# Kernel optimization log

Hardware: AMD Instinct MI355X
Metric: run time of the kernel (lower is better)

Reference implementation:

```python
import jax, jax.numpy as jnp
import numpy as np

DIM = 512
HEADS = 8
WIN = 64
HIDDEN = 2048
EPS = 1e-5


def layernorm(x, g, b):
    mu = jnp.mean(x, axis=-1, keepdims=True)
    var = jnp.var(x, axis=-1, keepdims=True)
    return (x - mu) * jax.lax.rsqrt(var + EPS) * g + b


def setup_inputs() -> dict:
    key = jax.random.key(0)
    ks = jax.random.split(key, 10)
    s = lambda fan_in: 1.0 / np.sqrt(fan_in)
    return {
        "x": jax.random.normal(ks[0], (8, 4096, DIM), dtype=jnp.float32),
        "ln1_g": jnp.ones((DIM,), jnp.float32),
        "ln1_b": jnp.zeros((DIM,), jnp.float32),
        "qkv_w": jax.random.normal(ks[1], (DIM, 3 * DIM), jnp.float32) * s(DIM),
        "qkv_b": jnp.zeros((3 * DIM,), jnp.float32),
        "proj_w": jax.random.normal(ks[2], (DIM, DIM), jnp.float32) * s(DIM),
        "proj_b": jnp.zeros((DIM,), jnp.float32),
        "ln2_g": jnp.ones((DIM,), jnp.float32),
        "ln2_b": jnp.zeros((DIM,), jnp.float32),
        "fc1_w": jax.random.normal(ks[3], (DIM, HIDDEN), jnp.float32) * s(DIM),
        "fc1_b": jnp.zeros((HIDDEN,), jnp.float32),
        "fc2_w": jax.random.normal(ks[4], (HIDDEN, DIM), jnp.float32) * s(HIDDEN),
        "fc2_b": jnp.zeros((DIM,), jnp.float32),
    }


def reference(x, ln1_g, ln1_b, qkv_w, qkv_b, proj_w, proj_b, ln2_g, ln2_b,
              fc1_w, fc1_b, fc2_w, fc2_b):
    B, N, C = x.shape
    hd = C // HEADS
    scale = hd ** -0.5

    # --- W-MSA (shift_size forced to 0, attn_mask None) ---
    h = layernorm(x, ln1_g, ln1_b)
    hw = h.reshape(B * (N // WIN), WIN, C)
    qkv = hw @ qkv_w + qkv_b
    qkv = qkv.reshape(-1, WIN, 3, HEADS, hd)
    q = qkv[:, :, 0] * scale
    k = qkv[:, :, 1]
    v = qkv[:, :, 2]
    attn = jnp.einsum('bqhd,bkhd->bhqk', q, k)
    attn = jax.nn.softmax(attn, axis=-1)
    o = jnp.einsum('bhqk,bkhd->bqhd', attn, v).reshape(-1, WIN, C)
    o = o @ proj_w + proj_b
    x = x + o.reshape(B, N, C)

    # --- MLP (GELU exact, dropout=0) ---
    h2 = layernorm(x, ln2_g, ln2_b)
    h2 = jax.nn.gelu(h2 @ fc1_w + fc1_b, approximate=False)
    x = x + (h2 @ fc2_w + fc2_b)
    return x
```

## Files before the change

### kernel.cpp

```cpp
#include <hip/hip_runtime.h>
#include <hip/hip_bf16.h>
#include <cstdint>

typedef unsigned short U16;
typedef float f32x4 __attribute__((ext_vector_type(4)));
typedef __bf16 bf16x8 __attribute__((ext_vector_type(8)));

#define DEVINL __device__ __forceinline__

DEVINL U16 f2bf(float f) {
    unsigned u = __float_as_uint(f);
    return (U16)((u + 0x7FFFu + ((u >> 16) & 1u)) >> 16);
}
DEVINL float bf2f(U16 s) { return __uint_as_float(((unsigned)s) << 16); }

DEVINL void gld16(const void* g, void* l) {
    __builtin_amdgcn_global_load_lds(
        (const __attribute__((address_space(1))) void*)g,
        (__attribute__((address_space(3))) void*)l, 16, 0, 0);
}

#define MFMA_BF16 __builtin_amdgcn_mfma_f32_16x16x32_bf16

__global__ __launch_bounds__(256) void tcast_kernel(const float* __restrict__ w,
                                                    U16* __restrict__ wt, int K, int N) {
    __shared__ float tile[32][33];
    int n0 = blockIdx.x * 32, k0 = blockIdx.y * 32;
    int tx = threadIdx.x, ty = threadIdx.y;
#pragma unroll
    for (int i = 0; i < 32; i += 8) tile[ty + i][tx] = w[(size_t)(k0 + ty + i) * N + (n0 + tx)];
    __syncthreads();
#pragma unroll
    for (int i = 0; i < 32; i += 8) wt[(size_t)(n0 + ty + i) * K + (k0 + tx)] = f2bf(tile[tx][ty + i]);
}

__global__ __launch_bounds__(256) void ln_kernel(const float* __restrict__ x,
                                                 const float* __restrict__ g,
                                                 const float* __restrict__ b,
                                                 U16* __restrict__ out) {
    int lane = threadIdx.x & 63;
    size_t row = (size_t)blockIdx.x * 4 + (threadIdx.x >> 6);
    const float4* xr = (const float4*)(x + row * 512);
    float4 v0 = xr[lane], v1 = xr[lane + 64];
    float s = (v0.x + v0.y) + (v0.z + v0.w) + (v1.x + v1.y) + (v1.z + v1.w);
    float sq = (v0.x * v0.x + v0.y * v0.y + v0.z * v0.z + v0.w * v0.w) +
               (v1.x * v1.x + v1.y * v1.y + v1.z * v1.z + v1.w * v1.w);
#pragma unroll
    for (int m = 1; m < 64; m <<= 1) { s += __shfl_xor(s, m); sq += __shfl_xor(sq, m); }
    float mu = s * (1.f / 512.f);
    float var = sq * (1.f / 512.f) - mu * mu;
    float rs = rsqrtf(var + 1e-5f);
    const float4* g4 = (const float4*)g;
    const float4* b4 = (const float4*)b;
    float4 gv = g4[lane], bv = b4[lane];
    ushort4 o;
    o.x = f2bf((v0.x - mu) * rs * gv.x + bv.x);
    o.y = f2bf((v0.y - mu) * rs * gv.y + bv.y);
    o.z = f2bf((v0.z - mu) * rs * gv.z + bv.z);
    o.w = f2bf((v0.w - mu) * rs * gv.w + bv.w);
    ((ushort4*)(out + row * 512))[lane] = o;
    gv = g4[lane + 64]; bv = b4[lane + 64];
    o.x = f2bf((v1.x - mu) * rs * gv.x + bv.x);
    o.y = f2bf((v1.y - mu) * rs * gv.y + bv.y);
    o.z = f2bf((v1.z - mu) * rs * gv.z + bv.z);
    o.w = f2bf((v1.w - mu) * rs * gv.w + bv.w);
    ((ushort4*)(out + row * 512))[lane + 64] = o;
}

template <int EPI, int K>
__global__ __launch_bounds__(256, 4) void gemm_rt(const U16* __restrict__ A,
                                                  const U16* __restrict__ Bt,
                                                  const float* __restrict__ bias,
                                                  const float* __restrict__ resid,
                                                  U16* __restrict__ outb,
                                                  float* __restrict__ outf,
                                                  int M, int N, int gridN) {
    __shared__ __align__(16) U16 smem[16384];

    const int tid = threadIdx.x;
    const int lane = tid & 63, wv = tid >> 6;
    const int lo = lane & 15, hi = lane >> 4;
    const int wm = wv >> 1, wn = wv & 1;

    const int nwg = gridDim.x, bid = blockIdx.x;
    const int swzb = (bid & 7) * (nwg >> 3) + (bid >> 3);
    const int bn = swzb % gridN, bm = swzb / gridN;

    const int sr = tid >> 2;
    const int lc = (tid & 3) ^ ((sr >> 1) & 3);
    const U16* gA0 = A + (size_t)(bm * 128 + sr) * K + lc * 8;
    const U16* gA1 = gA0 + (size_t)64 * K;
    const U16* gB0 = Bt + (size_t)(bn * 128 + sr) * K + lc * 8;
    const U16* gB1 = gB0 + (size_t)64 * K;

#define STAGE(t2)                                                     \
    do {                                                              \
        U16* _l = smem + ((t2) & 1) * 8192 + tid * 8;                 \
        gld16(gA0 + (t2) * 32, _l);                                   \
        gld16(gA1 + (t2) * 32, _l + 2048);                            \
        gld16(gB0 + (t2) * 32, _l + 4096);                            \
        gld16(gB1 + (t2) * 32, _l + 6144);                            \
    } while (0)

    const int ck = (hi ^ ((lo >> 1) & 3)) << 3;

    f32x4 acc[4][4] = {};

    constexpr int NT = K >> 5;
    static_assert(NT >= 16 && (NT % 16) == 0, "K must be a multiple of 512");

    STAGE(0);

    auto tile = [&](int t, bool pf) __attribute__((always_inline)) {
        if (pf) {
            STAGE(t + 1);
            asm volatile("s_waitcnt vmcnt(4)" ::: "memory");
        } else {
            asm volatile("s_waitcnt vmcnt(0)" ::: "memory");
        }
        __builtin_amdgcn_s_barrier();

        const int cb = (t & 1) * 8192;
        const U16* Ab = smem + cb + (wm * 64 + lo) * 32 + ck;
        const U16* Bb = smem + cb + 4096 + (wn * 64 + lo) * 32 + ck;

        bf16x8 af[4], bg[4];
#pragma unroll
        for (int i = 0; i < 4; ++i) af[i] = *(const bf16x8*)(Ab + i * 512);
#pragma unroll
        for (int j = 0; j < 4; ++j) bg[j] = *(const bf16x8*)(Bb + j * 512);

        __builtin_amdgcn_s_setprio(1);
#pragma unroll
        for (int i = 0; i < 4; ++i)
#pragma unroll
            for (int j = 0; j < 4; ++j)
                acc[i][j] = MFMA_BF16(af[i], bg[j], acc[i][j], 0, 0, 0);
        __builtin_amdgcn_s_setprio(0);
        __builtin_amdgcn_s_barrier();
    };

    for (int t0 = 0; t0 + 16 < NT; t0 += 16) {
#pragma unroll
        for (int tt = 0; tt < 16; ++tt) tile(t0 + tt, true);
    }
#pragma unroll
    for (int tt = 0; tt < 16; ++tt) {
        const int t = NT - 16 + tt;
        tile(t, t + 1 < NT);
    }

    const int row0 = bm * 128 + wm * 64 + hi * 4;
    const int col0 = bn * 128 + wn * 64 + lo;
    float bc[4];
#pragma unroll
    for (int j = 0; j < 4; ++j) bc[j] = bias[col0 + j * 16];

    if (EPI == 1) {
#pragma unroll
        for (int i = 0; i < 4; ++i)
#pragma unroll
            for (int r = 0; r < 4; ++r) {
                const size_t rowb = (size_t)(row0 + i * 16 + r) * N;
#pragma unroll
                for (int j = 0; j < 4; ++j) {
                    const size_t idx = rowb + col0 + j * 16;
                    outf[idx] = acc[i][j][r] + bc[j] + resid[idx];
                }
            }
    } else {
#pragma unroll
        for (int i = 0; i < 4; ++i)
#pragma unroll
            for (int j = 0; j < 4; ++j)
#pragma unroll
                for (int r = 0; r < 4; ++r) {
                    float v = acc[i][j][r] + bc[j];
                    if (EPI == 2) {
                        float u = v * (0.7978845608028654f + 0.0356774081f * v * v);
                        v = v / (1.f + __expf(-2.f * u));
                    }
                    outb[(size_t)(row0 + i * 16 + r) * N + col0 + j * 16] = f2bf(v);
                }
    }
#undef STAGE
}

__global__ __launch_bounds__(256) void attn_kernel(const U16* __restrict__ qkv,
                                                   U16* __restrict__ o) {
    const int blk = blockIdx.x;
    const int w = blk >> 3, h = blk & 7;
    const int tid = threadIdx.x;
    const int lane = tid & 63, wv = tid >> 6;
    const int lo = lane & 15, hi = lane >> 4;

    __shared__ __align__(16) U16 Qs[64][72];
    __shared__ __align__(16) U16 Ks[64][72];
    __shared__ __align__(16) U16 Vt[64][72];
    __shared__ __align__(16) U16 Ps[4][16][72];

    {
        const int r = tid >> 2;
        const int c0 = (tid & 3) << 4;
        const U16* p = qkv + (size_t)(w * 64 + r) * 1536 + h * 64 + c0;
        *(bf16x8*)&Ks[r][c0] = *(const bf16x8*)(p + 512);
        *(bf16x8*)&Ks[r][c0 + 8] = *(const bf16x8*)(p + 520);
        const U16* pv = p + 1024;
#pragma unroll
        for (int i = 0; i < 16; i++) Vt[c0 + i][r] = pv[i];
#pragma unroll
        for (int i = 0; i < 16; i++) Qs[r][c0 + i] = f2bf(bf2f(p[i]) * 0.125f);
    }
    __syncthreads();

    const int rb = wv * 16;
    f32x4 s[4] = {};
#pragma unroll
    for (int dc = 0; dc < 64; dc += 32) {
        bf16x8 a = *(const bf16x8*)&Qs[rb + lo][dc + hi * 8];
#pragma unroll
        for (int jb = 0; jb < 4; jb++) {
            bf16x8 bfr = *(const bf16x8*)&Ks[jb * 16 + lo][dc + hi * 8];
            s[jb] = MFMA_BF16(a, bfr, s[jb], 0, 0, 0);
        }
    }
#pragma unroll
    for (int r = 0; r < 4; r++) {
        float m = fmaxf(fmaxf(s[0][r], s[1][r]), fmaxf(s[2][r], s[3][r]));
#pragma unroll
        for (int msk = 1; msk < 16; msk <<= 1) m = fmaxf(m, __shfl_xor(m, msk));
        float e[4], sum = 0.f;
#pragma unroll
        for (int jb = 0; jb < 4; jb++) { e[jb] = expf(s[jb][r] - m); sum += e[jb]; }
#pragma unroll
        for (int msk = 1; msk < 16; msk <<= 1) sum += __shfl_xor(sum, msk);
        float inv = 1.f / sum;
#pragma unroll
        for (int jb = 0; jb < 4; jb++) Ps[wv][hi * 4 + r][jb * 16 + lo] = f2bf(e[jb] * inv);
    }
    __syncthreads();

    f32x4 oa[4] = {};
#pragma unroll
    for (int jc = 0; jc < 64; jc += 32) {
        bf16x8 a = *(const bf16x8*)&Ps[wv][lo][jc + hi * 8];
#pragma unroll
        for (int db = 0; db < 4; db++) {
            bf16x8 bfr = *(const bf16x8*)&Vt[db * 16 + lo][jc + hi * 8];
            oa[db] = MFMA_BF16(a, bfr, oa[db], 0, 0, 0);
        }
    }
#pragma unroll
    for (int db = 0; db < 4; db++)
#pragma unroll
        for (int r = 0; r < 4; r++)
            o[(size_t)(w * 64 + rb + hi * 4 + r) * 512 + h * 64 + db * 16 + lo] = f2bf(oa[db][r]);
}

extern "C" void kernel_launch(void* const* d_in, const int* in_sizes, int n_in,
                              void* d_out, int out_size, void* d_ws, size_t ws_size,
                              hipStream_t stream) {
    const float* x = (const float*)d_in[0];
    const float* ln1_g = (const float*)d_in[1];
    const float* ln1_b = (const float*)d_in[2];
    const float* qkv_w = (const float*)d_in[3];
    const float* qkv_b = (const float*)d_in[4];
    const float* proj_w = (const float*)d_in[5];
    const float* proj_b = (const float*)d_in[6];
    const float* ln2_g = (const float*)d_in[7];
    const float* ln2_b = (const float*)d_in[8];
    const float* fc1_w = (const float*)d_in[9];
    const float* fc1_b = (const float*)d_in[10];
    const float* fc2_w = (const float*)d_in[11];
    const float* fc2_b = (const float*)d_in[12];
    float* out = (float*)d_out;

    char* ws = (char*)d_ws;
    U16* hbuf = (U16*)ws;
    U16* big = (U16*)(ws + 33554432);
    U16* wt_qkv = (U16*)(ws + 33554432 + 134217728);
    U16* wt_proj = wt_qkv + 1536 * 512;
    U16* wt_fc1 = wt_proj + 512 * 512;
    U16* wt_fc2 = wt_fc1 + 2048 * 512;

    dim3 tb(32, 8);
    tcast_kernel<<<dim3(1536 / 32, 512 / 32), tb, 0, stream>>>(qkv_w, wt_qkv, 512, 1536);
    tcast_kernel<<<dim3(512 / 32, 512 / 32), tb, 0, stream>>>(proj_w, wt_proj, 512, 512);
    tcast_kernel<<<dim3(2048 / 32, 512 / 32), tb, 0, stream>>>(fc1_w, wt_fc1, 512, 2048);
    tcast_kernel<<<dim3(512 / 32, 2048 / 32), tb, 0, stream>>>(fc2_w, wt_fc2, 2048, 512);

    ln_kernel<<<8192, 256, 0, stream>>>(x, ln1_g, ln1_b, hbuf);
    gemm_rt<0, 512><<<3072, 256, 0, stream>>>(hbuf, wt_qkv, qkv_b, nullptr, big, nullptr, 32768, 1536, 12);
    attn_kernel<<<4096, 256, 0, stream>>>(big, hbuf);
    gemm_rt<1, 512><<<1024, 256, 0, stream>>>(hbuf, wt_proj, proj_b, x, nullptr, out, 32768, 512, 4);
    ln_kernel<<<8192, 256, 0, stream>>>(out, ln2_g, ln2_b, hbuf);
    gemm_rt<2, 512><<<4096, 256, 0, stream>>>(hbuf, wt_fc1, fc1_b, nullptr, big, nullptr, 32768, 2048, 16);
    gemm_rt<1, 2048><<<1024, 256, 0, stream>>>(big, wt_fc2, fc2_b, out, nullptr, out, 32768, 512, 4);
}
```

Measured before the change: 375.3 us.

## Double-buffer LDS fragment reads in GEMM to overlap with MFMA

Restructures the GEMM main loop so the LDS-to-register fragment loads for tile t+1 are issued before the MFMAs of tile t, using two register fragment sets. The global-to-LDS prefetch now runs two tiles ahead with a two-tile prologue. The goal is to hide LDS read latency behind matrix math. The extra fragment registers force launch bounds down from 4 to 3 waves per SIMD, which lowers occupancy.

```diff
diff --git a/kernel.cpp b/kernel.cpp
--- a/kernel.cpp
+++ b/kernel.cpp
@@ -68,7 +68,7 @@
 }
 
 template <int EPI, int K>
-__global__ __launch_bounds__(256, 4) void gemm_rt(const U16* __restrict__ A,
+__global__ __launch_bounds__(256, 3) void gemm_rt(const U16* __restrict__ A,
                                                   const U16* __restrict__ Bt,
                                                   const float* __restrict__ bias,
                                                   const float* __restrict__ resid,
@@ -93,61 +93,86 @@
     const U16* gB0 = Bt + (size_t)(bn * 128 + sr) * K + lc * 8;
     const U16* gB1 = gB0 + (size_t)64 * K;
 
-#define STAGE(t2)                                                     \
-    do {                                                              \
-        U16* _l = smem + ((t2) & 1) * 8192 + tid * 8;                 \
-        gld16(gA0 + (t2) * 32, _l);                                   \
-        gld16(gA1 + (t2) * 32, _l + 2048);                            \
-        gld16(gB0 + (t2) * 32, _l + 4096);                            \
-        gld16(gB1 + (t2) * 32, _l + 6144);                            \
+    const int ck = (hi ^ ((lo >> 1) & 3)) << 3;
+    const int aoff = (wm * 64 + lo) * 32 + ck;
+    const int boff = 4096 + (wn * 64 + lo) * 32 + ck;
+
+    f32x4 acc[4][4] = {};
+    bf16x8 afA[4], bgA[4], afB[4], bgB[4];
+
+#define RD(AF, BG, CB)                                                          \
+    do {                                                                        \
+        const U16* _Ab = smem + (CB) + aoff;                                    \
+        const U16* _Bb = smem + (CB) + boff;                                    \
+        _Pragma("unroll") for (int i = 0; i < 4; ++i)                           \
+            AF[i] = *(const bf16x8*)(_Ab + i * 512);                            \
+        _Pragma("unroll") for (int j = 0; j < 4; ++j)                           \
+            BG[j] = *(const bf16x8*)(_Bb + j * 512);                            \
     } while (0)
 
-    const int ck = (hi ^ ((lo >> 1) & 3)) << 3;
-
-    f32x4 acc[4][4] = {};
+#define MM(AF, BG)                                                              \
+    do {                                                                        \
+        __builtin_amdgcn_s_setprio(1);                                          \
+        _Pragma("unroll") for (int i = 0; i < 4; ++i)                           \
+            _Pragma("unroll") for (int j = 0; j < 4; ++j)                       \
+                acc[i][j] = MFMA_BF16(AF[i], BG[j], acc[i][j], 0, 0, 0);        \
+        __builtin_amdgcn_s_setprio(0);                                          \
+    } while (0)
+
+#define ITER(tt, TREL, LIM)                                                     \
+    do {                                                                        \
+        if ((TREL) + 2 < (LIM)) {                                               \
+            U16* _l = smem + (((tt)&1) ? 8192 : 0) + tid * 8;                   \
+            gld16(gAc0 + ((tt) + 2) * 32, _l);                                  \
+            gld16(gAc1 + ((tt) + 2) * 32, _l + 2048);                           \
+            gld16(gBc0 + ((tt) + 2) * 32, _l + 4096);                           \
+            gld16(gBc1 + ((tt) + 2) * 32, _l + 6144);                           \
+            asm volatile("s_waitcnt vmcnt(4)" ::: "memory");                    \
+        } else {                                                                \
+            asm volatile("s_waitcnt vmcnt(0)" ::: "memory");                    \
+        }                                                                       \
+        __builtin_amdgcn_s_barrier();                                           \
+        if ((TREL) + 1 < (LIM)) {                                               \
+            const int _cb = (((tt) + 1) & 1) ? 8192 : 0;                        \
+            if (((tt)&1) == 0) RD(afB, bgB, _cb); else RD(afA, bgA, _cb);       \
+        }                                                                       \
+        __builtin_amdgcn_sched_barrier(0x8);                                    \
+        if (((tt)&1) == 0) MM(afA, bgA); else MM(afB, bgB);                     \
+        asm volatile("s_waitcnt lgkmcnt(0)" ::: "memory");                      \
+        __builtin_amdgcn_s_barrier();                                           \
+    } while (0)
 
     constexpr int NT = K >> 5;
     static_assert(NT >= 16 && (NT % 16) == 0, "K must be a multiple of 512");
 
-    STAGE(0);
-
-    auto tile = [&](int t, bool pf) __attribute__((always_inline)) {
-        if (pf) {
-            STAGE(t + 1);
-            asm volatile("s_waitcnt vmcnt(4)" ::: "memory");
-        } else {
-            asm volatile("s_waitcnt vmcnt(0)" ::: "memory");
-        }
-        __builtin_amdgcn_s_barrier();
-
-        const int cb = (t & 1) * 8192;
-        const U16* Ab = smem + cb + (wm * 64 + lo) * 32 + ck;
-        const U16* Bb = smem + cb + 4096 + (wn * 64 + lo) * 32 + ck;
-
-        bf16x8 af[4], bg[4];
-#pragma unroll
-        for (int i = 0; i < 4; ++i) af[i] = *(const bf16x8*)(Ab + i * 512);
-#pragma unroll
-        for (int j = 0; j < 4; ++j) bg[j] = *(const bf16x8*)(Bb + j * 512);
-
-        __builtin_amdgcn_s_setprio(1);
-#pragma unroll
-        for (int i = 0; i < 4; ++i)
-#pragma unroll
-            for (int j = 0; j < 4; ++j)
-                acc[i][j] = MFMA_BF16(af[i], bg[j], acc[i][j], 0, 0, 0);
-        __builtin_amdgcn_s_setprio(0);
-        __builtin_amdgcn_s_barrier();
-    };
+    {
+        U16* _l = smem + tid * 8;
+        gld16(gA0, _l);          gld16(gA1, _l + 2048);
+        gld16(gB0, _l + 4096);   gld16(gB1, _l + 6144);
+        U16* _l2 = smem + 8192 + tid * 8;
+        gld16(gA0 + 32, _l2);        gld16(gA1 + 32, _l2 + 2048);
+        gld16(gB0 + 32, _l2 + 4096); gld16(gB1 + 32, _l2 + 6144);
+    }
+    asm volatile("s_waitcnt vmcnt(4)" ::: "memory");
+    __builtin_amdgcn_s_barrier();
+    RD(afA, bgA, 0);
 
     for (int t0 = 0; t0 + 16 < NT; t0 += 16) {
-#pragma unroll
-        for (int tt = 0; tt < 16; ++tt) tile(t0 + tt, true);
-    }
-#pragma unroll
-    for (int tt = 0; tt < 16; ++tt) {
-        const int t = NT - 16 + tt;
-        tile(t, t + 1 < NT);
+        const U16* gAc0 = gA0 + (size_t)t0 * 32;
+        const U16* gAc1 = gA1 + (size_t)t0 * 32;
+        const U16* gBc0 = gB0 + (size_t)t0 * 32;
+        const U16* gBc1 = gB1 + (size_t)t0 * 32;
+#pragma unroll
+        for (int tt = 0; tt < 16; ++tt) ITER(tt, tt, 1 << 30);
+    }
+    {
+        constexpr int t0 = NT - 16;
+        const U16* gAc0 = gA0 + (size_t)t0 * 32;
+        const U16* gAc1 = gA1 + (size_t)t0 * 32;
+        const U16* gBc0 = gB0 + (size_t)t0 * 32;
+        const U16* gBc1 = gB1 + (size_t)t0 * 32;
+#pragma unroll
+        for (int tt = 0; tt < 16; ++tt) ITER(tt, tt, 16);
     }
 
     const int row0 = bm * 128 + wm * 64 + hi * 4;
@@ -183,7 +208,9 @@
                     outb[(size_t)(row0 + i * 16 + r) * N + col0 + j * 16] = f2bf(v);
                 }
     }
-#undef STAGE
+#undef ITER
+#undef MM
+#undef RD
 }
 
 __global__ __launch_bounds__(256) void attn_kernel(const U16* __restrict__ qkv,
```

After: 377.5 us. About the same (+0.6%).

## Triple-buffer GEMM LDS tiles with one barrier per k-step; use fast exp

Applied to the files above, without the earlier changes.

Moves the GEMM main loop from double to triple LDS buffering. The next tile is issued two steps ahead, after the barrier, which removes the trailing barrier in each k-iteration. LDS per block grows from 32KB to 48KB, which may limit occupancy under the 4-blocks-per-SM launch bound. The attention softmax also switches expf to __expf, trading slight accuracy for fewer instructions.

```diff
diff --git a/kernel.cpp b/kernel.cpp
--- a/kernel.cpp
+++ b/kernel.cpp
@@ -75,7 +75,7 @@
                                                   U16* __restrict__ outb,
                                                   float* __restrict__ outf,
                                                   int M, int N, int gridN) {
-    __shared__ __align__(16) U16 smem[16384];
+    __shared__ __align__(16) U16 smem[24576];
 
     const int tid = threadIdx.x;
     const int lane = tid & 63, wv = tid >> 6;
@@ -95,7 +95,7 @@
 
 #define STAGE(t2)                                                     \
     do {                                                              \
-        U16* _l = smem + ((t2) & 1) * 8192 + tid * 8;                 \
+        U16* _l = smem + ((t2) % 3) * 8192 + tid * 8;                 \
         gld16(gA0 + (t2) * 32, _l);                                   \
         gld16(gA1 + (t2) * 32, _l + 2048);                            \
         gld16(gB0 + (t2) * 32, _l + 4096);                            \
@@ -103,6 +103,8 @@
     } while (0)
 
     const int ck = (hi ^ ((lo >> 1) & 3)) << 3;
+    const int aoff = (wm * 64 + lo) * 32 + ck;
+    const int boff = 4096 + (wn * 64 + lo) * 32 + ck;
 
     f32x4 acc[4][4] = {};
 
@@ -110,44 +112,38 @@
     static_assert(NT >= 16 && (NT % 16) == 0, "K must be a multiple of 512");
 
     STAGE(0);
-
-    auto tile = [&](int t, bool pf) __attribute__((always_inline)) {
-        if (pf) {
-            STAGE(t + 1);
-            asm volatile("s_waitcnt vmcnt(4)" ::: "memory");
-        } else {
-            asm volatile("s_waitcnt vmcnt(0)" ::: "memory");
-        }
-        __builtin_amdgcn_s_barrier();
-
-        const int cb = (t & 1) * 8192;
-        const U16* Ab = smem + cb + (wm * 64 + lo) * 32 + ck;
-        const U16* Bb = smem + cb + 4096 + (wn * 64 + lo) * 32 + ck;
-
-        bf16x8 af[4], bg[4];
-#pragma unroll
-        for (int i = 0; i < 4; ++i) af[i] = *(const bf16x8*)(Ab + i * 512);
-#pragma unroll
-        for (int j = 0; j < 4; ++j) bg[j] = *(const bf16x8*)(Bb + j * 512);
-
-        __builtin_amdgcn_s_setprio(1);
-#pragma unroll
-        for (int i = 0; i < 4; ++i)
-#pragma unroll
-            for (int j = 0; j < 4; ++j)
-                acc[i][j] = MFMA_BF16(af[i], bg[j], acc[i][j], 0, 0, 0);
-        __builtin_amdgcn_s_setprio(0);
-        __builtin_amdgcn_s_barrier();
-    };
-
-    for (int t0 = 0; t0 + 16 < NT; t0 += 16) {
-#pragma unroll
-        for (int tt = 0; tt < 16; ++tt) tile(t0 + tt, true);
-    }
-#pragma unroll
-    for (int tt = 0; tt < 16; ++tt) {
-        const int t = NT - 16 + tt;
-        tile(t, t + 1 < NT);
+    STAGE(1);
+
+#define ITER(t)                                                                 \
+    do {                                                                        \
+        if ((t) + 1 < NT) {                                                     \
+            asm volatile("s_waitcnt vmcnt(4)" ::: "memory");                    \
+        } else {                                                                \
+            asm volatile("s_waitcnt vmcnt(0)" ::: "memory");                    \
+        }                                                                       \
+        __builtin_amdgcn_s_barrier();                                           \
+        if ((t) + 2 < NT) STAGE((t) + 2);                                       \
+        {                                                                       \
+            const int _cb = ((t) % 3) * 8192;                                   \
+            const U16* _Ab = smem + _cb + aoff;                                 \
+            const U16* _Bb = smem + _cb + boff;                                 \
+            bf16x8 af[4], bg[4];                                                \
+            _Pragma("unroll") for (int i = 0; i < 4; ++i)                       \
+                af[i] = *(const bf16x8*)(_Ab + i * 512);                        \
+            _Pragma("unroll") for (int j = 0; j < 4; ++j)                       \
+                bg[j] = *(const bf16x8*)(_Bb + j * 512);                        \
+            __builtin_amdgcn_s_setprio(1);                                      \
+            _Pragma("unroll") for (int i = 0; i < 4; ++i)                       \
+                _Pragma("unroll") for (int j = 0; j < 4; ++j)                   \
+                    acc[i][j] = MFMA_BF16(af[i], bg[j], acc[i][j], 0, 0, 0);    \
+            __builtin_amdgcn_s_setprio(0);                                      \
+        }                                                                       \
+    } while (0)
+
+#pragma unroll
+    for (int t0 = 0; t0 < NT; t0 += 16) {
+#pragma unroll
+        for (int tt = 0; tt < 16; ++tt) ITER(t0 + tt);
     }
 
     const int row0 = bm * 128 + wm * 64 + hi * 4;
@@ -183,6 +179,7 @@
                     outb[(size_t)(row0 + i * 16 + r) * N + col0 + j * 16] = f2bf(v);
                 }
     }
+#undef ITER
 #undef STAGE
 }
 
@@ -231,7 +228,7 @@
         for (int msk = 1; msk < 16; msk <<= 1) m = fmaxf(m, __shfl_xor(m, msk));
         float e[4], sum = 0.f;
 #pragma unroll
-        for (int jb = 0; jb < 4; jb++) { e[jb] = expf(s[jb][r] - m); sum += e[jb]; }
+        for (int jb = 0; jb < 4; jb++) { e[jb] = __expf(s[jb][r] - m); sum += e[jb]; }
 #pragma unroll
         for (int msk = 1; msk < 16; msk <<= 1) sum += __shfl_xor(sum, msk);
         float inv = 1.f / sum;
```

After: 380.5 us. No clear change (+1.4%).
